# Kernel tuning notes

Measured on AMD Instinct MI355X. Metric: run time of the kernel, lower is better.

The kernel has to match this reference:

```python
import jax, jax.numpy as jnp
import numpy as np

N_GAUSS = 1000
H, W = 512, 512
CHUNK = 100  # gaussians per scan step; peak intermediate CHUNK*H*W floats


def setup_inputs() -> dict:
    key = jax.random.key(0)
    k1, k2, k3, k4 = jax.random.split(key, 4)
    return {
        "positions": jax.random.uniform(k1, (N_GAUSS, 2), dtype=jnp.float32),
        "scales": jax.random.uniform(k2, (N_GAUSS, 2), dtype=jnp.float32),
        "rotations": jax.random.normal(k3, (N_GAUSS,), dtype=jnp.float32),
        "colors": jax.random.uniform(k4, (N_GAUSS, 3), dtype=jnp.float32),
        "opacities": jnp.ones((N_GAUSS,), dtype=jnp.float32),
    }


def _render(positions, scales, rotations, colors, opacities):
    y = jnp.linspace(0.0, 1.0, H, dtype=positions.dtype)
    x = jnp.linspace(0.0, 1.0, W, dtype=positions.dtype)
    gy, gx = jnp.meshgrid(y, x, indexing="ij")  # [H,W]

    n = positions.shape[0]
    n_chunks = n // CHUNK

    def body(img, args):
        pos, sc, rot, col, op = args  # pos [C,2], sc [C,2], rot [C], col [C,3], op [C]
        cos_r = jnp.cos(rot)[:, None, None]
        sin_r = jnp.sin(rot)[:, None, None]
        dx = gx[None] - pos[:, 0, None, None]  # [C,H,W]
        dy = gy[None] - pos[:, 1, None, None]
        x_rot = cos_r * dx + sin_r * dy
        y_rot = -sin_r * dx + cos_r * dy
        s = jnp.abs(sc) + 1e-6
        g = jnp.exp(-0.5 * ((x_rot / s[:, 0, None, None]) ** 2
                            + (y_rot / s[:, 1, None, None]) ** 2))
        alpha = g * jax.nn.sigmoid(op)[:, None, None]  # [C,H,W]
        img = img + jnp.einsum("nhw,nc->chw", alpha, jax.nn.sigmoid(col))
        return img, None

    chunks = tuple(a.reshape(n_chunks, CHUNK, *a.shape[1:])
                   for a in (positions, scales, rotations, colors, opacities))
    img0 = jnp.zeros((3, H, W), dtype=positions.dtype)
    img, _ = jax.lax.scan(body, img0, chunks)
    return jnp.clip(img, 0.0, 1.0)


def reference(positions, scales, rotations, colors, opacities):
    return _render(positions, scales, rotations, colors, opacities)
```

## Files before the change

kernel.cpp:

```cpp
#include <hip/hip_runtime.h>
#include <math.h>

#define HH 512
#define WW 512
#define NG 1000
#define NCH 125
#define STEP (1.0f / 511.0f)

#define SAT_THR 1.10f

#define SCH_BIAS 1064986823.0f
#define SCALE23 2896.309376f

__device__ __forceinline__ float clamp01(float v) {
    return fminf(fmaxf(v, 0.0f), 1.0f);
}

__device__ __forceinline__ float bits2e(float s) {
    return __uint_as_float((unsigned int)s);
}

__global__ __launch_bounds__(256) void gs_fused(
        const float* __restrict__ pos,
        const float* __restrict__ sc,
        const float* __restrict__ rot,
        const float* __restrict__ col,
        const float* __restrict__ op,
        float* __restrict__ out) {
    __shared__ __align__(16) float sD[NCH][6][8];

    const int tid  = threadIdx.x;
    const int row  = blockIdx.x >> 1;
    const int colb = (blockIdx.x & 1) << 8;
    const float y  = (float)row * STEP;
    const float xb = (float)colb * STEP;
    const float K = 0.84932180f;

    for (int g = tid; g < NG; g += 256) {
        const float px = pos[2 * g + 0];
        const float py = pos[2 * g + 1];
        const float sx = fabsf(sc[2 * g + 0]) + 1e-6f;
        const float sy = fabsf(sc[2 * g + 1]) + 1e-6f;
        const float r  = rot[g];
        const float cth = __cosf(r);
        const float sth = __sinf(r);
        const float isx = SCALE23 * K / sx;
        const float isy = SCALE23 * K / sy;
        const float rxx = cth * isx;
        const float rxy = sth * isx;
        const float ryx = -sth * isy;
        const float ryy = cth * isy;
        const float ox = rxx * px + rxy * py;
        const float oy = ryx * px + ryy * py;
        const float a0 = fmaf(rxx, xb, fmaf(rxy, y, -ox));
        const float b0 = fmaf(ryx, xb, fmaf(ryy, y, -oy));
        const float da = rxx * STEP;
        const float db = ryx * STEP;
        const float s0 = fmaf(-a0, a0, fmaf(-b0, b0, SCH_BIAS));
        const float c1 = -2.0f * fmaf(a0, da, b0 * db);
        const float c2 = -fmaf(da, da, db * db);
        const float so = 1.0f / (1.0f + __expf(-op[g]));
        const float cr = so / (1.0f + __expf(-col[3 * g + 0]));
        const float cg = so / (1.0f + __expf(-col[3 * g + 1]));
        const float cb = so / (1.0f + __expf(-col[3 * g + 2]));
        const int ch = g >> 3;
        const int k  = g & 7;
        sD[ch][0][k] = s0;
        sD[ch][1][k] = c1;
        sD[ch][2][k] = c2;
        sD[ch][3][k] = cr;
        sD[ch][4][k] = cg;
        sD[ch][5][k] = cb;
    }
    __syncthreads();

    const float t  = (float)tid;
    const float t2 = t * t;

    float aR = 0.f, aG = 0.f, aB = 0.f;

    for (int ch = 0; ch < NCH; ++ch) {
        const float4 S0a = *(const float4*)&sD[ch][0][0];
        const float4 S0b = *(const float4*)&sD[ch][0][4];
        const float4 C1a = *(const float4*)&sD[ch][1][0];
        const float4 C1b = *(const float4*)&sD[ch][1][4];
        const float4 C2a = *(const float4*)&sD[ch][2][0];
        const float4 C2b = *(const float4*)&sD[ch][2][4];
        const float4 CRa = *(const float4*)&sD[ch][3][0];
        const float4 CRb = *(const float4*)&sD[ch][3][4];
        const float4 CGa = *(const float4*)&sD[ch][4][0];
        const float4 CGb = *(const float4*)&sD[ch][4][4];
        const float4 CBa = *(const float4*)&sD[ch][5][0];
        const float4 CBb = *(const float4*)&sD[ch][5][4];

#define ACC(S0, C1, C2, CR, CG, CB)                                  \
        {                                                            \
            const float e = bits2e(fmaf(t2, (C2), fmaf(t, (C1), (S0)))); \
            aR = fmaf(e, (CR), aR);                                  \
            aG = fmaf(e, (CG), aG);                                  \
            aB = fmaf(e, (CB), aB);                                  \
        }
        ACC(S0a.x, C1a.x, C2a.x, CRa.x, CGa.x, CBa.x)
        ACC(S0a.y, C1a.y, C2a.y, CRa.y, CGa.y, CBa.y)
        ACC(S0a.z, C1a.z, C2a.z, CRa.z, CGa.z, CBa.z)
        ACC(S0a.w, C1a.w, C2a.w, CRa.w, CGa.w, CBa.w)
        ACC(S0b.x, C1b.x, C2b.x, CRb.x, CGb.x, CBb.x)
        ACC(S0b.y, C1b.y, C2b.y, CRb.y, CGb.y, CBb.y)
        ACC(S0b.z, C1b.z, C2b.z, CRb.z, CGb.z, CBb.z)
        ACC(S0b.w, C1b.w, C2b.w, CRb.w, CGb.w, CBb.w)
#undef ACC

        if (__all(fminf(fminf(aR, aG), aB) > SAT_THR)) {
            break;
        }
    }

    const int idx = row * WW + colb + tid;
    const int hw = HH * WW;
    out[0 * hw + idx] = clamp01(aR);
    out[1 * hw + idx] = clamp01(aG);
    out[2 * hw + idx] = clamp01(aB);
}

extern "C" void kernel_launch(void* const* d_in, const int* in_sizes, int n_in,
                              void* d_out, int out_size, void* d_ws, size_t ws_size,
                              hipStream_t stream) {
    const float* pos = (const float*)d_in[0];
    const float* sc  = (const float*)d_in[1];
    const float* rot = (const float*)d_in[2];
    const float* col = (const float*)d_in[3];
    const float* op  = (const float*)d_in[4];
    float* out = (float*)d_out;

    gs_fused<<<HH * 2, 256, 0, stream>>>(pos, sc, rot, col, op, out);
}
```

Before: 11.18 us.

## Use full-row 512-thread blocks and double-buffer shared chunk loads

Each block now renders a full image row with 512 threads instead of half a row with 256, halving the number of blocks that redo the per-gaussian setup into shared memory. The inner loop is software-pipelined: the next chunk's coefficients are loaded into registers while the current chunk is accumulated, with the shared array padded by two chunks for the lookahead. This raises register pressure and reduces block count, which may lower occupancy.

```diff
diff --git a/kernel.cpp b/kernel.cpp
--- a/kernel.cpp
+++ b/kernel.cpp
@@ -20,23 +20,21 @@
     return __uint_as_float((unsigned int)s);
 }
 
-__global__ __launch_bounds__(256) void gs_fused(
+__global__ __launch_bounds__(512, 4) void gs_fused(
         const float* __restrict__ pos,
         const float* __restrict__ sc,
         const float* __restrict__ rot,
         const float* __restrict__ col,
         const float* __restrict__ op,
         float* __restrict__ out) {
-    __shared__ __align__(16) float sD[NCH][6][8];
+    __shared__ __align__(16) float sD[NCH + 2][6][8];
 
-    const int tid  = threadIdx.x;
-    const int row  = blockIdx.x >> 1;
-    const int colb = (blockIdx.x & 1) << 8;
-    const float y  = (float)row * STEP;
-    const float xb = (float)colb * STEP;
+    const int tid = threadIdx.x;
+    const int row = blockIdx.x;
+    const float y = (float)row * STEP;
     const float K = 0.84932180f;
 
-    for (int g = tid; g < NG; g += 256) {
+    for (int g = tid; g < NG; g += 512) {
         const float px = pos[2 * g + 0];
         const float py = pos[2 * g + 1];
         const float sx = fabsf(sc[2 * g + 0]) + 1e-6f;
@@ -52,8 +50,8 @@
         const float ryy = cth * isy;
         const float ox = rxx * px + rxy * py;
         const float oy = ryx * px + ryy * py;
-        const float a0 = fmaf(rxx, xb, fmaf(rxy, y, -ox));
-        const float b0 = fmaf(ryx, xb, fmaf(ryy, y, -oy));
+        const float a0 = fmaf(rxy, y, -ox);
+        const float b0 = fmaf(ryy, y, -oy);
         const float da = rxx * STEP;
         const float db = ryx * STEP;
         const float s0 = fmaf(-a0, a0, fmaf(-b0, b0, SCH_BIAS));
@@ -79,43 +77,59 @@
 
     float aR = 0.f, aG = 0.f, aB = 0.f;
 
-    for (int ch = 0; ch < NCH; ++ch) {
-        const float4 S0a = *(const float4*)&sD[ch][0][0];
-        const float4 S0b = *(const float4*)&sD[ch][0][4];
-        const float4 C1a = *(const float4*)&sD[ch][1][0];
-        const float4 C1b = *(const float4*)&sD[ch][1][4];
-        const float4 C2a = *(const float4*)&sD[ch][2][0];
-        const float4 C2b = *(const float4*)&sD[ch][2][4];
-        const float4 CRa = *(const float4*)&sD[ch][3][0];
-        const float4 CRb = *(const float4*)&sD[ch][3][4];
-        const float4 CGa = *(const float4*)&sD[ch][4][0];
-        const float4 CGb = *(const float4*)&sD[ch][4][4];
-        const float4 CBa = *(const float4*)&sD[ch][5][0];
-        const float4 CBb = *(const float4*)&sD[ch][5][4];
+#define LOADCH(P, ch)                                  \
+    P##S0a = *(const float4*)&sD[ch][0][0];            \
+    P##S0b = *(const float4*)&sD[ch][0][4];            \
+    P##C1a = *(const float4*)&sD[ch][1][0];            \
+    P##C1b = *(const float4*)&sD[ch][1][4];            \
+    P##C2a = *(const float4*)&sD[ch][2][0];            \
+    P##C2b = *(const float4*)&sD[ch][2][4];            \
+    P##CRa = *(const float4*)&sD[ch][3][0];            \
+    P##CRb = *(const float4*)&sD[ch][3][4];            \
+    P##CGa = *(const float4*)&sD[ch][4][0];            \
+    P##CGb = *(const float4*)&sD[ch][4][4];            \
+    P##CBa = *(const float4*)&sD[ch][5][0];            \
+    P##CBb = *(const float4*)&sD[ch][5][4];
 
-#define ACC(S0, C1, C2, CR, CG, CB)                                  \
-        {                                                            \
-            const float e = bits2e(fmaf(t2, (C2), fmaf(t, (C1), (S0)))); \
-            aR = fmaf(e, (CR), aR);                                  \
-            aG = fmaf(e, (CG), aG);                                  \
-            aB = fmaf(e, (CB), aB);                                  \
+#define ACC1(S0, C1, C2, CR, CG, CB)                                   \
+    {                                                                  \
+        const float e = bits2e(fmaf(t2, (C2), fmaf(t, (C1), (S0))));   \
+        aR = fmaf(e, (CR), aR);                                        \
+        aG = fmaf(e, (CG), aG);                                        \
+        aB = fmaf(e, (CB), aB);                                        \
+    }
+
+#define ACC8(P)                                                        \
+    ACC1(P##S0a.x, P##C1a.x, P##C2a.x, P##CRa.x, P##CGa.x, P##CBa.x)   \
+    ACC1(P##S0a.y, P##C1a.y, P##C2a.y, P##CRa.y, P##CGa.y, P##CBa.y)   \
+    ACC1(P##S0a.z, P##C1a.z, P##C2a.z, P##CRa.z, P##CGa.z, P##CBa.z)   \
+    ACC1(P##S0a.w, P##C1a.w, P##C2a.w, P##CRa.w, P##CGa.w, P##CBa.w)   \
+    ACC1(P##S0b.x, P##C1b.x, P##C2b.x, P##CRb.x, P##CGb.x, P##CBb.x)   \
+    ACC1(P##S0b.y, P##C1b.y, P##C2b.y, P##CRb.y, P##CGb.y, P##CBb.y)   \
+    ACC1(P##S0b.z, P##C1b.z, P##C2b.z, P##CRb.z, P##CGb.z, P##CBb.z)   \
+    ACC1(P##S0b.w, P##C1b.w, P##C2b.w, P##CRb.w, P##CGb.w, P##CBb.w)
+
+    float4 aS0a, aS0b, aC1a, aC1b, aC2a, aC2b, aCRa, aCRb, aCGa, aCGb, aCBa, aCBb;
+    float4 bS0a, bS0b, bC1a, bC1b, bC2a, bC2b, bCRa, bCRb, bCGa, bCGb, bCBa, bCBb;
+
+    LOADCH(a, 0)
+    for (int ch = 0; ch < NCH; ch += 2) {
+        LOADCH(b, ch + 1)
+        ACC8(a)
+        if (__all(fminf(fminf(aR, aG), aB) > SAT_THR) || ch + 1 >= NCH) {
+            break;
         }
-        ACC(S0a.x, C1a.x, C2a.x, CRa.x, CGa.x, CBa.x)
-        ACC(S0a.y, C1a.y, C2a.y, CRa.y, CGa.y, CBa.y)
-        ACC(S0a.z, C1a.z, C2a.z, CRa.z, CGa.z, CBa.z)
-        ACC(S0a.w, C1a.w, C2a.w, CRa.w, CGa.w, CBa.w)
-        ACC(S0b.x, C1b.x, C2b.x, CRb.x, CGb.x, CBb.x)
-        ACC(S0b.y, C1b.y, C2b.y, CRb.y, CGb.y, CBb.y)
-        ACC(S0b.z, C1b.z, C2b.z, CRb.z, CGb.z, CBb.z)
-        ACC(S0b.w, C1b.w, C2b.w, CRb.w, CGb.w, CBb.w)
-#undef ACC
-
+        LOADCH(a, ch + 2)
+        ACC8(b)
         if (__all(fminf(fminf(aR, aG), aB) > SAT_THR)) {
             break;
         }
     }
+#undef ACC8
+#undef ACC1
+#undef LOADCH
 
-    const int idx = row * WW + colb + tid;
+    const int idx = row * WW + tid;
     const int hw = HH * WW;
     out[0 * hw + idx] = clamp01(aR);
     out[1 * hw + idx] = clamp01(aG);
@@ -132,5 +146,5 @@
     const float* op  = (const float*)d_in[4];
     float* out = (float*)d_out;
 
-    gs_fused<<<HH * 2, 256, 0, stream>>>(pos, sc, rot, col, op, out);
+    gs_fused<<<HH, 512, 0, stream>>>(pos, sc, rot, col, op, out);
 }
```

Result: faster. 9.881 us (-11.6%).
